# Performance work log

Hardware: AMD Instinct MI355X
Metric: run time of the kernel (lower is better)

The kernel has to match this reference:

```python
import jax, jax.numpy as jnp
import numpy as np

N_NODES = 100000
N_EDGES = 3200000
D = 64
DROPOUT_P = 0.1

# LBSign: sign forward, straight-through clamped gradient backward
@jax.custom_vjp
def sign_ste(x):
    return jnp.sign(x)

def _sign_fwd(x):
    return jnp.sign(x), None

def _sign_bwd(_, g):
    return (jnp.clip(g, -1.0, 1.0),)

sign_ste.defvjp(_sign_fwd, _sign_bwd)


def hsgcn(x, src, dst, n):
    # HSGCN layer: add self-loops, degree-normalized mean aggregation, sign STE
    loop = jnp.arange(n)
    src_sl = jnp.concatenate([src, loop])  # [E+N]
    dst_sl = jnp.concatenate([dst, loop])  # [E+N]
    deg = jax.ops.segment_sum(jnp.ones(src_sl.shape[0], x.dtype), dst_sl, num_segments=n)  # [N]
    agg = jax.ops.segment_sum(x[src_sl], dst_sl, num_segments=n)  # [N, D]
    return sign_ste(agg / deg[:, None])


def setup_inputs() -> dict:
    key = jax.random.key(0)
    k1, k2 = jax.random.split(key)
    x = jax.random.normal(k1, (N_NODES, D), dtype=jnp.float32)
    edge_index = jax.random.randint(k2, (2, N_EDGES), 0, N_NODES, dtype=jnp.int64)
    return {"x": x, "edge_index": edge_index}


def reference(x, edge_index):
    src, dst = edge_index[0], edge_index[1]
    x = jnp.tanh(x)
    h_0 = x                      # training=True path
    h = sign_ste(x)
    h_1 = hsgcn(h_0, src, dst, N_NODES)
    h_2 = hsgcn(h_1, src, dst, N_NODES)
    # dropout p=0.1, deterministic fixed-key mask (training mode)
    keep = jax.random.bernoulli(jax.random.key(42), 1.0 - DROPOUT_P, h_2.shape)
    h_2 = jnp.where(keep, h_2 / (1.0 - DROPOUT_P), 0.0)
    return (h, h_2)
```

## Files before the change

kernel.cpp:

```cpp
#include <hip/hip_runtime.h>

#define NN 100000
#define NE 3200000
#define DD 64

constexpr int ELEMS = NN * DD;
constexpr int NBK   = (NN + 255) / 256;
constexpr int NBLK  = 512;
constexpr int EPB   = NE / NBLK;

__device__ __forceinline__ void threefry2x32_0_42(unsigned int c0, unsigned int c1,
                                                  unsigned int& o0, unsigned int& o1) {
  const unsigned int ks0 = 0u;
  const unsigned int ks1 = 42u;
  const unsigned int ks2 = ks0 ^ ks1 ^ 0x1BD11BDAu;
  unsigned int x0 = c0 + ks0;
  unsigned int x1 = c1 + ks1;
#define TF_R(r) { x0 += x1; x1 = (x1 << (r)) | (x1 >> (32 - (r))); x1 ^= x0; }
  TF_R(13) TF_R(15) TF_R(26) TF_R(6)
  x0 += ks1; x1 += ks2 + 1u;
  TF_R(17) TF_R(29) TF_R(16) TF_R(24)
  x0 += ks2; x1 += ks0 + 2u;
  TF_R(13) TF_R(15) TF_R(26) TF_R(6)
  x0 += ks0; x1 += ks1 + 3u;
  TF_R(17) TF_R(29) TF_R(16) TF_R(24)
  x0 += ks1; x1 += ks2 + 4u;
  TF_R(13) TF_R(15) TF_R(26) TF_R(6)
  x0 += ks2; x1 += ks0 + 5u;
#undef TF_R
  o0 = x0; o1 = x1;
}

__device__ __forceinline__ bool keep_from_bits(unsigned int bits) {
  float f = __uint_as_float((bits >> 9) | 0x3f800000u) - 1.0f;
  return f < 0.9f;
}

__global__ void kA(const float* __restrict__ x,
                   float* __restrict__ h_out,
                   float* __restrict__ h0f) {
  int i = blockIdx.x * blockDim.x + threadIdx.x;
  if (i >= ELEMS) return;
  float xv = x[i];
  h0f[i] = (float)tanh((double)xv);
  h_out[i] = (xv > 0.0f) ? 1.0f : ((xv < 0.0f) ? -1.0f : 0.0f);
}

__global__ void k_cnt(const int* __restrict__ dst, int* __restrict__ counts) {
  __shared__ int c[NBK];
  int blk = blockIdx.x, t = threadIdx.x;
  for (int i = t; i < NBK; i += blockDim.x) c[i] = 0;
  __syncthreads();
  int e0 = blk * EPB;
  for (int e = e0 + t; e < e0 + EPB; e += blockDim.x)
    atomicAdd(&c[dst[e] >> 8], 1);
  __syncthreads();
  for (int i = t; i < NBK; i += blockDim.x) counts[i * NBLK + blk] = c[i];
}

__global__ void k_bofs(const int* __restrict__ counts,
                       int* __restrict__ offs_local, int* __restrict__ btot) {
  __shared__ int s[NBLK];
  int b = blockIdx.x, t = threadIdx.x;
  int own = counts[b * NBLK + t];
  s[t] = own;
  __syncthreads();
  for (int off = 1; off < NBLK; off <<= 1) {
    int add = (t >= off) ? s[t - off] : 0;
    __syncthreads();
    s[t] += add;
    __syncthreads();
  }
  offs_local[b * NBLK + t] = s[t] - own;
  if (t == NBLK - 1) btot[b] = s[t];
}

__global__ void k_bbase(const int* __restrict__ btot, int* __restrict__ bbase) {
  __shared__ int s[NBLK];
  int t = threadIdx.x;
  int own = (t < NBK) ? btot[t] : 0;
  s[t] = own;
  __syncthreads();
  for (int off = 1; off < NBLK; off <<= 1) {
    int add = (t >= off) ? s[t - off] : 0;
    __syncthreads();
    s[t] += add;
    __syncthreads();
  }
  if (t < NBK) bbase[t] = s[t] - own;
  if (t == 0) bbase[NBK] = NE;
}

__global__ void __launch_bounds__(512) k_bwrite(const int* __restrict__ src,
                                                const int* __restrict__ dst,
                                                const int* __restrict__ offs_local,
                                                const int* __restrict__ bbase,
                                                unsigned int* __restrict__ ebuf) {
  __shared__ unsigned int stage[EPB];
  __shared__ unsigned short bstage[EPB];
  __shared__ int cnt[NBK];
  __shared__ int sc[NBLK];
  __shared__ int cur[NBK];
  __shared__ int obase[NBK];
  int blk = blockIdx.x, t = threadIdx.x;
  int e0 = blk * EPB;

  for (int i = t; i < NBK; i += blockDim.x) cnt[i] = 0;
  __syncthreads();
  for (int e = e0 + t; e < e0 + EPB; e += blockDim.x)
    atomicAdd(&cnt[dst[e] >> 8], 1);
  __syncthreads();
  int own = (t < NBK) ? cnt[t] : 0;
  sc[t] = own;
  __syncthreads();
  for (int off = 1; off < NBLK; off <<= 1) {
    int add = (t >= off) ? sc[t - off] : 0;
    __syncthreads();
    sc[t] += add;
    __syncthreads();
  }
  if (t < NBK) {
    cur[t] = sc[t] - own;
    obase[t] = bbase[t] + offs_local[t * NBLK + blk];
  }
  __syncthreads();
  for (int e = e0 + t; e < e0 + EPB; e += blockDim.x) {
    int d = dst[e];
    int b = d >> 8;
    int p = atomicAdd(&cur[b], 1);
    stage[p] = ((unsigned int)src[e] << 8) | (unsigned int)(d & 255);
    bstage[p] = (unsigned short)b;
  }
  __syncthreads();
  for (int i = t; i < EPB; i += blockDim.x) {
    int b = (int)bstage[i];
    int local_excl = sc[b] - cnt[b];
    ebuf[obase[b] + (i - local_excl)] = stage[i];
  }
}

__global__ void k_fill(const int* __restrict__ bbase, const unsigned int* __restrict__ ebuf,
                       int* __restrict__ rowptr, int* __restrict__ csr_src) {
  __shared__ int cnt[256];
  __shared__ int sc[256];
  __shared__ int cur[256];
  int b = blockIdx.x;
  int t = threadIdx.x;
  int seg_beg = bbase[b];
  int seg_end = bbase[b + 1];
  int nfirst = b << 8;
  int ncount = min(256, NN - nfirst);

  cnt[t] = 0;
  __syncthreads();
  for (int j = seg_beg + t; j < seg_end; j += 256)
    atomicAdd(&cnt[ebuf[j] & 255u], 1);
  __syncthreads();
  int own = cnt[t];
  sc[t] = own;
  __syncthreads();
  for (int off = 1; off < 256; off <<= 1) {
    int add = (t >= off) ? sc[t - off] : 0;
    __syncthreads();
    sc[t] += add;
    __syncthreads();
  }
  if (t < ncount) {
    rowptr[nfirst + t + 1] = seg_beg + sc[t];
    cur[t] = seg_beg + sc[t] - own;
  }
  if (b == 0 && t == 0) rowptr[0] = 0;
  __syncthreads();
  for (int j = seg_beg + t; j < seg_end; j += 256) {
    unsigned int v = ebuf[j];
    int pos = atomicAdd(&cur[v & 255u], 1);
    csr_src[pos] = (int)(v >> 8);
  }
}

__global__ void k_gather1(const int* __restrict__ rowptr, const int* __restrict__ csr_src,
                          const float* __restrict__ h0f, signed char* __restrict__ h1) {
  int g = blockIdx.x * blockDim.x + threadIdx.x;
  int n = g >> 6;
  int lane = g & 63;
  if (n >= NN) return;
  int beg = rowptr[n], end = rowptr[n + 1];
  double acc = (double)h0f[n * DD + lane];
  int j = beg;
  for (; j + 4 <= end; j += 4) {
    int s0 = csr_src[j], s1 = csr_src[j + 1], s2 = csr_src[j + 2], s3 = csr_src[j + 3];
    float v0 = h0f[s0 * DD + lane];
    float v1 = h0f[s1 * DD + lane];
    float v2 = h0f[s2 * DD + lane];
    float v3 = h0f[s3 * DD + lane];
    acc += (double)v0; acc += (double)v1; acc += (double)v2; acc += (double)v3;
  }
  for (; j < end; ++j) acc += (double)h0f[csr_src[j] * DD + lane];
  h1[n * DD + lane] = (acc > 0.0) ? 1 : ((acc < 0.0) ? -1 : 0);
}

__global__ void k_gather2(const int* __restrict__ rowptr, const int* __restrict__ csr_src,
                          const signed char* __restrict__ h1, float* __restrict__ out2) {
  int g = blockIdx.x * blockDim.x + threadIdx.x;
  int n = g >> 6;
  int lane = g & 63;
  if (n >= NN) return;
  int beg = rowptr[n], end = rowptr[n + 1];
  int acc = (int)h1[n * DD + lane];
  int j = beg;
  for (; j + 4 <= end; j += 4) {
    int s0 = csr_src[j], s1 = csr_src[j + 1], s2 = csr_src[j + 2], s3 = csr_src[j + 3];
    acc += (int)h1[s0 * DD + lane] + (int)h1[s1 * DD + lane]
         + (int)h1[s2 * DD + lane] + (int)h1[s3 * DD + lane];
  }
  for (; j < end; ++j) acc += (int)h1[csr_src[j] * DD + lane];

  int i = n * DD + lane;
  float s = (acc > 0) ? 1.0f : ((acc < 0) ? -1.0f : 0.0f);
  unsigned int o0, o1;
  threefry2x32_0_42(0u, (unsigned int)i, o0, o1);
  unsigned int bits = o0 ^ o1;
  const float inv_keep = 1.0f / 0.9f;
  out2[i] = keep_from_bits(bits) ? s * inv_keep : 0.0f;
}

extern "C" void kernel_launch(void* const* d_in, const int* in_sizes, int n_in,
                              void* d_out, int out_size, void* d_ws, size_t ws_size,
                              hipStream_t stream) {
  const float* x   = (const float*)d_in[0];
  const int*   ei  = (const int*)d_in[1];
  const int*   src = ei;
  const int*   dst = ei + NE;

  float* out_h  = (float*)d_out;
  float* out_h2 = (float*)d_out + ELEMS;

  char* ws = (char*)d_ws;
  float*        h0f        = (float*)ws;
  signed char*  h1         = (signed char*)(ws + ((size_t)26 << 20));
  int*          rowptr     = (int*)(ws + ((size_t)33 << 20));
  int*          bbase      = (int*)(ws + ((size_t)34 << 20));
  int*          btot       = (int*)(ws + ((size_t)35 << 20));
  int*          counts     = (int*)(ws + ((size_t)36 << 20));
  int*          offs_local = (int*)(ws + ((size_t)37 << 20));
  int*          csr_src    = (int*)(ws + ((size_t)38 << 20));
  unsigned int* ebuf       = (unsigned int*)(ws + ((size_t)51 << 20));

  const int B = 256;
  const int gElems = (ELEMS + B - 1) / B;

  kA<<<gElems, B, 0, stream>>>(x, out_h, h0f);

  k_cnt<<<NBLK, B, 0, stream>>>(dst, counts);
  k_bofs<<<NBK, NBLK, 0, stream>>>(counts, offs_local, btot);
  k_bbase<<<1, NBLK, 0, stream>>>(btot, bbase);
  k_bwrite<<<NBLK, NBLK, 0, stream>>>(src, dst, offs_local, bbase, ebuf);
  k_fill<<<NBK, B, 0, stream>>>(bbase, ebuf, rowptr, csr_src);

  k_gather1<<<gElems, B, 0, stream>>>(rowptr, csr_src, h0f, h1);
  k_gather2<<<gElems, B, 0, stream>>>(rowptr, csr_src, h1, out_h2);
}
```

Measured before the change: 374.2 us.

## Bit-pack layer-1 signs via wave ballot and merge elementwise init with edge count

Layer-1 sign outputs are stored as two 64-bit ballot masks (positive and negative) per node instead of one int8 per feature. Each gathered neighbour row then shrinks from 64 bytes to 16 bytes in the second aggregation. The tanh/sign elementwise kernel is also merged into the edge-counting kernel as extra blocks, removing one launch and letting the two overlap. The cost is per-lane bit extraction, and the ballot relies on a 64-wide wavefront mapping one node to one wave.

```diff
diff --git a/kernel.cpp b/kernel.cpp
--- a/kernel.cpp
+++ b/kernel.cpp
@@ -36,26 +36,28 @@
   return f < 0.9f;
 }
 
-__global__ void kA(const float* __restrict__ x,
-                   float* __restrict__ h_out,
-                   float* __restrict__ h0f) {
-  int i = blockIdx.x * blockDim.x + threadIdx.x;
-  if (i >= ELEMS) return;
-  float xv = x[i];
-  h0f[i] = (float)tanh((double)xv);
-  h_out[i] = (xv > 0.0f) ? 1.0f : ((xv < 0.0f) ? -1.0f : 0.0f);
-}
-
-__global__ void k_cnt(const int* __restrict__ dst, int* __restrict__ counts) {
+__global__ void k_init(const float* __restrict__ x,
+                       float* __restrict__ h_out,
+                       float* __restrict__ h0f,
+                       const int* __restrict__ dst,
+                       int* __restrict__ counts) {
   __shared__ int c[NBK];
-  int blk = blockIdx.x, t = threadIdx.x;
-  for (int i = t; i < NBK; i += blockDim.x) c[i] = 0;
-  __syncthreads();
-  int e0 = blk * EPB;
-  for (int e = e0 + t; e < e0 + EPB; e += blockDim.x)
-    atomicAdd(&c[dst[e] >> 8], 1);
-  __syncthreads();
-  for (int i = t; i < NBK; i += blockDim.x) counts[i * NBLK + blk] = c[i];
+  if (blockIdx.x < NBLK) {
+    int blk = blockIdx.x, t = threadIdx.x;
+    for (int i = t; i < NBK; i += blockDim.x) c[i] = 0;
+    __syncthreads();
+    int e0 = blk * EPB;
+    for (int e = e0 + t; e < e0 + EPB; e += blockDim.x)
+      atomicAdd(&c[dst[e] >> 8], 1);
+    __syncthreads();
+    for (int i = t; i < NBK; i += blockDim.x) counts[i * NBLK + blk] = c[i];
+  } else {
+    int i = (blockIdx.x - NBLK) * blockDim.x + threadIdx.x;
+    if (i >= ELEMS) return;
+    float xv = x[i];
+    h0f[i] = (float)tanh((double)xv);
+    h_out[i] = (xv > 0.0f) ? 1.0f : ((xv < 0.0f) ? -1.0f : 0.0f);
+  }
 }
 
 __global__ void k_bofs(const int* __restrict__ counts,
@@ -179,7 +181,7 @@
 }
 
 __global__ void k_gather1(const int* __restrict__ rowptr, const int* __restrict__ csr_src,
-                          const float* __restrict__ h0f, signed char* __restrict__ h1) {
+                          const float* __restrict__ h0f, ulonglong2* __restrict__ pp) {
   int g = blockIdx.x * blockDim.x + threadIdx.x;
   int n = g >> 6;
   int lane = g & 63;
@@ -196,24 +198,39 @@
     acc += (double)v0; acc += (double)v1; acc += (double)v2; acc += (double)v3;
   }
   for (; j < end; ++j) acc += (double)h0f[csr_src[j] * DD + lane];
-  h1[n * DD + lane] = (acc > 0.0) ? 1 : ((acc < 0.0) ? -1 : 0);
+  unsigned long long bp = __ballot(acc > 0.0);
+  unsigned long long bn = __ballot(acc < 0.0);
+  if (lane == 0) {
+    ulonglong2 v; v.x = bp; v.y = bn;
+    pp[n] = v;
+  }
 }
 
 __global__ void k_gather2(const int* __restrict__ rowptr, const int* __restrict__ csr_src,
-                          const signed char* __restrict__ h1, float* __restrict__ out2) {
+                          const ulonglong2* __restrict__ pp, float* __restrict__ out2) {
   int g = blockIdx.x * blockDim.x + threadIdx.x;
   int n = g >> 6;
   int lane = g & 63;
   if (n >= NN) return;
   int beg = rowptr[n], end = rowptr[n + 1];
-  int acc = (int)h1[n * DD + lane];
+  ulonglong2 ps = pp[n];
+  int acc = (int)((ps.x >> lane) & 1ull) - (int)((ps.y >> lane) & 1ull);
   int j = beg;
   for (; j + 4 <= end; j += 4) {
     int s0 = csr_src[j], s1 = csr_src[j + 1], s2 = csr_src[j + 2], s3 = csr_src[j + 3];
-    acc += (int)h1[s0 * DD + lane] + (int)h1[s1 * DD + lane]
-         + (int)h1[s2 * DD + lane] + (int)h1[s3 * DD + lane];
-  }
-  for (; j < end; ++j) acc += (int)h1[csr_src[j] * DD + lane];
+    ulonglong2 p0 = pp[s0];
+    ulonglong2 p1 = pp[s1];
+    ulonglong2 p2 = pp[s2];
+    ulonglong2 p3 = pp[s3];
+    acc += (int)((p0.x >> lane) & 1ull) - (int)((p0.y >> lane) & 1ull);
+    acc += (int)((p1.x >> lane) & 1ull) - (int)((p1.y >> lane) & 1ull);
+    acc += (int)((p2.x >> lane) & 1ull) - (int)((p2.y >> lane) & 1ull);
+    acc += (int)((p3.x >> lane) & 1ull) - (int)((p3.y >> lane) & 1ull);
+  }
+  for (; j < end; ++j) {
+    ulonglong2 p = pp[csr_src[j]];
+    acc += (int)((p.x >> lane) & 1ull) - (int)((p.y >> lane) & 1ull);
+  }
 
   int i = n * DD + lane;
   float s = (acc > 0) ? 1.0f : ((acc < 0) ? -1.0f : 0.0f);
@@ -237,26 +254,24 @@
 
   char* ws = (char*)d_ws;
   float*        h0f        = (float*)ws;
-  signed char*  h1         = (signed char*)(ws + ((size_t)26 << 20));
-  int*          rowptr     = (int*)(ws + ((size_t)33 << 20));
-  int*          bbase      = (int*)(ws + ((size_t)34 << 20));
-  int*          btot       = (int*)(ws + ((size_t)35 << 20));
-  int*          counts     = (int*)(ws + ((size_t)36 << 20));
-  int*          offs_local = (int*)(ws + ((size_t)37 << 20));
-  int*          csr_src    = (int*)(ws + ((size_t)38 << 20));
-  unsigned int* ebuf       = (unsigned int*)(ws + ((size_t)51 << 20));
+  ulonglong2*   pp         = (ulonglong2*)(ws + ((size_t)26 << 20));
+  int*          rowptr     = (int*)(ws + ((size_t)28 << 20));
+  int*          bbase      = (int*)(ws + ((size_t)29 << 20));
+  int*          btot       = (int*)(ws + ((size_t)30 << 20));
+  int*          counts     = (int*)(ws + ((size_t)31 << 20));
+  int*          offs_local = (int*)(ws + ((size_t)32 << 20));
+  int*          csr_src    = (int*)(ws + ((size_t)33 << 20));
+  unsigned int* ebuf       = (unsigned int*)(ws + ((size_t)46 << 20));
 
   const int B = 256;
   const int gElems = (ELEMS + B - 1) / B;
 
-  kA<<<gElems, B, 0, stream>>>(x, out_h, h0f);
-
-  k_cnt<<<NBLK, B, 0, stream>>>(dst, counts);
+  k_init<<<NBLK + gElems, B, 0, stream>>>(x, out_h, h0f, dst, counts);
   k_bofs<<<NBK, NBLK, 0, stream>>>(counts, offs_local, btot);
   k_bbase<<<1, NBLK, 0, stream>>>(btot, bbase);
   k_bwrite<<<NBLK, NBLK, 0, stream>>>(src, dst, offs_local, bbase, ebuf);
   k_fill<<<NBK, B, 0, stream>>>(bbase, ebuf, rowptr, csr_src);
 
-  k_gather1<<<gElems, B, 0, stream>>>(rowptr, csr_src, h0f, h1);
-  k_gather2<<<gElems, B, 0, stream>>>(rowptr, csr_src, h1, out_h2);
-}
+  k_gather1<<<gElems, B, 0, stream>>>(rowptr, csr_src, h0f, pp);
+  k_gather2<<<gElems, B, 0, stream>>>(rowptr, csr_src, pp, out_h2);
+}
```

After: 411.1 us. 9.8% more time.
